# Kernel tuning notes

Measured on AMD Instinct MI355X. Metric: run time of the kernel, lower is better.

The kernel has to match this reference:

```python
import math
import jax, jax.numpy as jnp
import numpy as np

HIDDEN = 768
N_SIGNALS = 15
DIM = HIDDEN // 4  # 192
B, S = 32, 4096


def setup_inputs() -> dict:
    key = jax.random.key(0)
    ks = jax.random.split(key, 11)
    return {
        "token_embeds": jax.random.normal(ks[0], (B, S, HIDDEN), jnp.float32),
        "Wk": jax.random.normal(ks[1], (HIDDEN, DIM), jnp.float32) * 0.02,
        "bk": jax.random.normal(ks[2], (DIM,), jnp.float32) * 0.02,
        "Wv": jax.random.normal(ks[3], (HIDDEN, DIM), jnp.float32) * 0.02,
        "bv": jax.random.normal(ks[4], (DIM,), jnp.float32) * 0.02,
        "signal_queries": jax.random.normal(ks[5], (N_SIGNALS, DIM), jnp.float32),
        "null_embeddings": jax.random.normal(ks[6], (N_SIGNALS, HIDDEN), jnp.float32) * 0.01,
        "W1": jax.random.normal(ks[7], (2 * DIM, 64), jnp.float32) * 0.05,
        "b1": jax.random.normal(ks[8], (64,), jnp.float32) * 0.05,
        "W2": jax.random.normal(ks[9], (64, 1), jnp.float32) * 0.05,
        "b2": jax.random.normal(ks[10], (1,), jnp.float32) * 0.05,
    }


def reference(token_embeds, Wk, bk, Wv, bv, signal_queries, null_embeddings, W1, b1, W2, b2):
    b, s, h = token_embeds.shape
    d = Wk.shape[1]
    # detect_signals: cross-attention from signal queries to tokens
    keys = token_embeds @ Wk + bk        # [B,S,d]
    values = token_embeds @ Wv + bv      # [B,S,d]
    scale = jnp.sqrt(jnp.float32(d))
    attn = jnp.einsum("nd,bsd->bns", signal_queries, keys) / scale  # [B,N,S]
    attn_weights = jax.nn.softmax(attn, axis=-1)
    signal_embeds = jnp.einsum("bns,bsd->bnd", attn_weights, values)  # [B,N,d]
    entropy = -(attn_weights * jnp.log(attn_weights + 1e-10)).sum(-1)  # [B,N]
    strength = 1.0 - entropy / jnp.float32(math.log(s))
    # estimate_causal_effects: batched over the 15 signals (original loops in Python)
    null_proj = jnp.broadcast_to(null_embeddings[:, :d], (b, null_embeddings.shape[0], d))
    eff_in = jnp.concatenate([signal_embeds, null_proj], axis=-1)  # [B,N,2d]
    hdn = jax.nn.gelu(eff_in @ W1 + b1, approximate=False)
    effects = (hdn @ W2 + b2)[..., 0]  # [B,N]
    # package (effects, strength) as one array [B, 2N]
    return jnp.concatenate([effects, strength], axis=-1)
```

## Files before the change

### kernel.cpp

```cpp
#include <hip/hip_runtime.h>
#include <math.h>

#define HID   768
#define DIMD  192
#define NSIG  15
#define BB    32
#define SS    4096
#define INV_SCALE 0.07216878364870322f
#define LOG_S     8.31776616671934f
#define NCHUNK 16
#define SC     256

#define WS_QK    ((size_t)0)
#define WS_QB    (WS_QK + NSIG*HID)
#define WS_ATTN  (WS_QB + 64)
#define WS_M     (WS_ATTN + (size_t)BB*NSIG*SS)
#define WS_INVL  (WS_M + BB*NSIG)
#define WS_CTXP  (WS_INVL + BB*NSIG)

__global__ __launch_bounds__(256) void k_qk(const float* __restrict__ q,
                                            const float* __restrict__ Wk,
                                            const float* __restrict__ bk,
                                            float* __restrict__ ws) {
  int idx = blockIdx.x * 256 + threadIdx.x;
  if (idx < NSIG * HID) {
    int n = idx / HID, h = idx - n * HID;
    const float* qr = q + n * DIMD;
    const float* wr = Wk + h * DIMD;
    float s = 0.f;
    #pragma unroll 4
    for (int d = 0; d < DIMD; ++d) s = fmaf(qr[d], wr[d], s);
    ws[WS_QK + (size_t)n * HID + h] = s * INV_SCALE;
  }
  if (idx < NSIG) {
    const float* qr = q + idx * DIMD;
    float s = 0.f;
    for (int d = 0; d < DIMD; ++d) s = fmaf(qr[d], bk[d], s);
    ws[WS_QB + idx] = s * INV_SCALE;
  }
}

#define HC 16
__global__ __launch_bounds__(256) void k_logits(const float* __restrict__ X,
                                                const float* __restrict__ ws_qk,
                                                const float* __restrict__ ws_qb,
                                                float* __restrict__ attn) {
  __shared__ float Qs[NSIG * HID];
  __shared__ float Xs[256 * (HC + 1)];
  const int t  = threadIdx.x;
  const int s0 = blockIdx.x * 256;
  const int b  = blockIdx.y;

  #pragma unroll
  for (int k = 0; k < (NSIG * HID) / 256; ++k)
    Qs[t + k * 256] = ws_qk[t + k * 256];

  float acc[NSIG];
  #pragma unroll
  for (int n = 0; n < NSIG; ++n) acc[n] = ws_qb[n];

  const float* Xb = X + ((size_t)(b * SS + s0)) * HID;

  for (int c = 0; c < HID / HC; ++c) {
    __syncthreads();
    #pragma unroll
    for (int k = 0; k < 4; ++k) {
      int j  = t + k * 256;
      int r  = j >> 2, cc = j & 3;
      float4 xv = *(const float4*)(Xb + (size_t)r * HID + c * HC + cc * 4);
      float* dst = Xs + r * (HC + 1) + cc * 4;
      dst[0] = xv.x; dst[1] = xv.y; dst[2] = xv.z; dst[3] = xv.w;
    }
    __syncthreads();
    const float* xrow = Xs + t * (HC + 1);
    #pragma unroll
    for (int c4 = 0; c4 < HC / 4; ++c4) {
      float x0 = xrow[c4*4+0], x1 = xrow[c4*4+1], x2 = xrow[c4*4+2], x3 = xrow[c4*4+3];
      #pragma unroll
      for (int n = 0; n < NSIG; ++n) {
        float4 qv = *(const float4*)(Qs + n * HID + c * HC + c4 * 4);
        acc[n] = fmaf(x0, qv.x, acc[n]);
        acc[n] = fmaf(x1, qv.y, acc[n]);
        acc[n] = fmaf(x2, qv.z, acc[n]);
        acc[n] = fmaf(x3, qv.w, acc[n]);
      }
    }
  }
  #pragma unroll
  for (int n = 0; n < NSIG; ++n)
    attn[((size_t)(b * NSIG + n)) * SS + s0 + t] = acc[n];
}

__global__ __launch_bounds__(256) void k_softmax_stats(const float* __restrict__ attn,
                                                       float* __restrict__ m_out,
                                                       float* __restrict__ invl_out,
                                                       float* __restrict__ out) {
  const int blk = blockIdx.x;
  const int b = blk / NSIG, n = blk - b * NSIG;
  const float* row = attn + ((size_t)(b * NSIG + n)) * SS;
  const int t = threadIdx.x;
  __shared__ float red[8];

  float m = -1e30f;
  for (int i = t; i < SS; i += 256) m = fmaxf(m, row[i]);
  #pragma unroll
  for (int o = 32; o > 0; o >>= 1) m = fmaxf(m, __shfl_down(m, o, 64));
  if ((t & 63) == 0) red[t >> 6] = m;
  __syncthreads();
  m = fmaxf(fmaxf(red[0], red[1]), fmaxf(red[2], red[3]));

  float l = 0.f, pa = 0.f;
  for (int i = t; i < SS; i += 256) {
    float a = row[i];
    float e = expf(a - m);
    l += e; pa = fmaf(e, a, pa);
  }
  #pragma unroll
  for (int o = 32; o > 0; o >>= 1) { l += __shfl_down(l, o, 64); pa += __shfl_down(pa, o, 64); }
  __syncthreads();
  if ((t & 63) == 0) { red[t >> 6] = l; red[4 + (t >> 6)] = pa; }
  __syncthreads();
  if (t == 0) {
    float L  = red[0] + red[1] + red[2] + red[3];
    float PA = red[4] + red[5] + red[6] + red[7];
    float entropy = m + logf(L) - PA / L;
    m_out[blk]    = m;
    invl_out[blk] = 1.f / L;
    out[b * (2 * NSIG) + NSIG + n] = 1.f - entropy / LOG_S;
  }
}

__global__ __launch_bounds__(256) void k_ctx(const float* __restrict__ X,
                                             const float* __restrict__ attn,
                                             const float* __restrict__ m_arr,
                                             const float* __restrict__ invl_arr,
                                             float* __restrict__ ctxp) {
  __shared__ float wLDS[NSIG * SC];
  const int t = threadIdx.x;
  const int chunk = blockIdx.x, b = blockIdx.y;
  const int s0 = chunk * SC;

  #pragma unroll
  for (int n = 0; n < NSIG; ++n) {
    float a = attn[((size_t)(b * NSIG + n)) * SS + s0 + t];
    wLDS[n * SC + t] = expf(a - m_arr[b * NSIG + n]) * invl_arr[b * NSIG + n];
  }
  __syncthreads();

  float acc[NSIG * 3];
  #pragma unroll
  for (int i = 0; i < NSIG * 3; ++i) acc[i] = 0.f;

  const float* Xb = X + ((size_t)(b * SS + s0)) * HID + t;
  for (int s = 0; s < SC; s += 4) {
    float x[12];
    #pragma unroll
    for (int j = 0; j < 4; ++j)
      #pragma unroll
      for (int k = 0; k < 3; ++k)
        x[j * 3 + k] = Xb[(size_t)(s + j) * HID + k * 256];
    #pragma unroll
    for (int n = 0; n < NSIG; ++n) {
      float4 wv = *(const float4*)(wLDS + n * SC + s);
      float wa[4] = {wv.x, wv.y, wv.z, wv.w};
      #pragma unroll
      for (int j = 0; j < 4; ++j)
        #pragma unroll
        for (int k = 0; k < 3; ++k)
          acc[n * 3 + k] = fmaf(wa[j], x[j * 3 + k], acc[n * 3 + k]);
    }
  }
  float* dst = ctxp + ((size_t)((b * NCHUNK + chunk) * NSIG)) * HID;
  #pragma unroll
  for (int n = 0; n < NSIG; ++n)
    #pragma unroll
    for (int k = 0; k < 3; ++k)
      dst[(size_t)n * HID + k * 256 + t] = acc[n * 3 + k];
}

__global__ __launch_bounds__(256) void k_final(const float* __restrict__ ctxp,
                                               const float* __restrict__ Wv,
                                               const float* __restrict__ bv,
                                               const float* __restrict__ nullemb,
                                               const float* __restrict__ W1,
                                               const float* __restrict__ b1,
                                               const float* __restrict__ W2,
                                               const float* __restrict__ b2,
                                               float* __restrict__ out) {
  const int blk = blockIdx.x;
  const int b = blk / NSIG, n = blk - b * NSIG;
  const int t = threadIdx.x;
  __shared__ float ctx[HID];
  __shared__ float se[DIMD];

  #pragma unroll
  for (int k = 0; k < 3; ++k) {
    int h = t + k * 256;
    float s = 0.f;
    #pragma unroll 4
    for (int c = 0; c < NCHUNK; ++c)
      s += ctxp[((size_t)((b * NCHUNK + c) * NSIG + n)) * HID + h];
    ctx[h] = s;
  }
  __syncthreads();
  if (t < DIMD) {
    float s = bv[t];
    #pragma unroll 4
    for (int h = 0; h < HID; ++h)
      s = fmaf(ctx[h], Wv[(size_t)h * DIMD + t], s);
    se[t] = s;
  }
  __syncthreads();
  if (t < 64) {
    float s = b1[t];
    const float* nrow = nullemb + (size_t)n * HID;
    #pragma unroll 4
    for (int i = 0; i < DIMD; ++i) s = fmaf(se[i],   W1[(size_t)i * 64 + t], s);
    #pragma unroll 4
    for (int i = 0; i < DIMD; ++i) s = fmaf(nrow[i], W1[(size_t)(DIMD + i) * 64 + t], s);
    float g = 0.5f * s * (1.f + erff(s * 0.70710678118654752f));
    float val = g * W2[t];
    #pragma unroll
    for (int o = 32; o > 0; o >>= 1) val += __shfl_down(val, o, 64);
    if (t == 0) out[b * (2 * NSIG) + n] = val + b2[0];
  }
}

extern "C" void kernel_launch(void* const* d_in, const int* in_sizes, int n_in,
                              void* d_out, int out_size, void* d_ws, size_t ws_size,
                              hipStream_t stream) {
  const float* X   = (const float*)d_in[0];
  const float* Wk  = (const float*)d_in[1];
  const float* bk  = (const float*)d_in[2];
  const float* Wv  = (const float*)d_in[3];
  const float* bv  = (const float*)d_in[4];
  const float* q   = (const float*)d_in[5];
  const float* nul = (const float*)d_in[6];
  const float* W1  = (const float*)d_in[7];
  const float* b1  = (const float*)d_in[8];
  const float* W2  = (const float*)d_in[9];
  const float* b2  = (const float*)d_in[10];
  float* out = (float*)d_out;
  float* ws  = (float*)d_ws;

  hipLaunchKernelGGL(k_qk, dim3(45), dim3(256), 0, stream, q, Wk, bk, ws);
  hipLaunchKernelGGL(k_logits, dim3(SS / 256, BB), dim3(256), 0, stream,
                     X, ws + WS_QK, ws + WS_QB, ws + WS_ATTN);
  hipLaunchKernelGGL(k_softmax_stats, dim3(BB * NSIG), dim3(256), 0, stream,
                     ws + WS_ATTN, ws + WS_M, ws + WS_INVL, out);
  hipLaunchKernelGGL(k_ctx, dim3(NCHUNK, BB), dim3(256), 0, stream,
                     X, ws + WS_ATTN, ws + WS_M, ws + WS_INVL, ws + WS_CTXP);
  hipLaunchKernelGGL(k_final, dim3(BB * NSIG), dim3(256), 0, stream,
                     ws + WS_CTXP, Wv, bv, nul, W1, b1, W2, b2, out);
}
```

Measured before the change: 876.1 us.

## Fuse logits, softmax and context into one flash-style chunked kernel

Merges the logits, softmax-statistics and weighted-context kernels into a single kernel per (chunk, batch). Each chunk keeps its logits in registers and shared memory, computes local max/sum/entropy partials, and writes unnormalised partial contexts. The final kernel rescales the partials with an online-softmax combine. This removes the global attention-logit buffer round trip and two launches, and lets X for a chunk be reused from cache between the two passes. In exchange, the Q matrix is now read straight from global/cache rather than staged in shared memory, and the grid is limited to 512 blocks.

```diff
diff --git a/kernel.cpp b/kernel.cpp
--- a/kernel.cpp
+++ b/kernel.cpp
@@ -6,17 +6,16 @@
 #define NSIG  15
 #define BB    32
 #define SS    4096
+#define SC    256
+#define NCHUNK (SS / SC)
+#define HC    32
 #define INV_SCALE 0.07216878364870322f
 #define LOG_S     8.31776616671934f
-#define NCHUNK 16
-#define SC     256
-
-#define WS_QK    ((size_t)0)
-#define WS_QB    (WS_QK + NSIG*HID)
-#define WS_ATTN  (WS_QB + 64)
-#define WS_M     (WS_ATTN + (size_t)BB*NSIG*SS)
-#define WS_INVL  (WS_M + BB*NSIG)
-#define WS_CTXP  (WS_INVL + BB*NSIG)
+
+#define WS_QK   ((size_t)0)
+#define WS_QB   (WS_QK + NSIG * HID)
+#define WS_ST   (WS_QB + 16)
+#define WS_CTXP (WS_ST + (size_t)BB * NCHUNK * NSIG * 3)
 
 __global__ __launch_bounds__(256) void k_qk(const float* __restrict__ q,
                                             const float* __restrict__ Wk,
@@ -40,145 +39,117 @@
   }
 }
 
-#define HC 16
-__global__ __launch_bounds__(256) void k_logits(const float* __restrict__ X,
-                                                const float* __restrict__ ws_qk,
-                                                const float* __restrict__ ws_qb,
-                                                float* __restrict__ attn) {
-  __shared__ float Qs[NSIG * HID];
-  __shared__ float Xs[256 * (HC + 1)];
-  const int t  = threadIdx.x;
-  const int s0 = blockIdx.x * 256;
-  const int b  = blockIdx.y;
-
-  #pragma unroll
-  for (int k = 0; k < (NSIG * HID) / 256; ++k)
-    Qs[t + k * 256] = ws_qk[t + k * 256];
-
-  float acc[NSIG];
-  #pragma unroll
-  for (int n = 0; n < NSIG; ++n) acc[n] = ws_qb[n];
-
-  const float* Xb = X + ((size_t)(b * SS + s0)) * HID;
-
-  for (int c = 0; c < HID / HC; ++c) {
-    __syncthreads();
-    #pragma unroll
-    for (int k = 0; k < 4; ++k) {
-      int j  = t + k * 256;
-      int r  = j >> 2, cc = j & 3;
-      float4 xv = *(const float4*)(Xb + (size_t)r * HID + c * HC + cc * 4);
-      float* dst = Xs + r * (HC + 1) + cc * 4;
-      dst[0] = xv.x; dst[1] = xv.y; dst[2] = xv.z; dst[3] = xv.w;
-    }
-    __syncthreads();
-    const float* xrow = Xs + t * (HC + 1);
-    #pragma unroll
-    for (int c4 = 0; c4 < HC / 4; ++c4) {
-      float x0 = xrow[c4*4+0], x1 = xrow[c4*4+1], x2 = xrow[c4*4+2], x3 = xrow[c4*4+3];
-      #pragma unroll
-      for (int n = 0; n < NSIG; ++n) {
-        float4 qv = *(const float4*)(Qs + n * HID + c * HC + c4 * 4);
-        acc[n] = fmaf(x0, qv.x, acc[n]);
-        acc[n] = fmaf(x1, qv.y, acc[n]);
-        acc[n] = fmaf(x2, qv.z, acc[n]);
-        acc[n] = fmaf(x3, qv.w, acc[n]);
-      }
-    }
-  }
-  #pragma unroll
-  for (int n = 0; n < NSIG; ++n)
-    attn[((size_t)(b * NSIG + n)) * SS + s0 + t] = acc[n];
-}
-
-__global__ __launch_bounds__(256) void k_softmax_stats(const float* __restrict__ attn,
-                                                       float* __restrict__ m_out,
-                                                       float* __restrict__ invl_out,
-                                                       float* __restrict__ out) {
-  const int blk = blockIdx.x;
-  const int b = blk / NSIG, n = blk - b * NSIG;
-  const float* row = attn + ((size_t)(b * NSIG + n)) * SS;
-  const int t = threadIdx.x;
-  __shared__ float red[8];
-
-  float m = -1e30f;
-  for (int i = t; i < SS; i += 256) m = fmaxf(m, row[i]);
-  #pragma unroll
-  for (int o = 32; o > 0; o >>= 1) m = fmaxf(m, __shfl_down(m, o, 64));
-  if ((t & 63) == 0) red[t >> 6] = m;
-  __syncthreads();
-  m = fmaxf(fmaxf(red[0], red[1]), fmaxf(red[2], red[3]));
-
-  float l = 0.f, pa = 0.f;
-  for (int i = t; i < SS; i += 256) {
-    float a = row[i];
-    float e = expf(a - m);
-    l += e; pa = fmaf(e, a, pa);
-  }
-  #pragma unroll
-  for (int o = 32; o > 0; o >>= 1) { l += __shfl_down(l, o, 64); pa += __shfl_down(pa, o, 64); }
-  __syncthreads();
-  if ((t & 63) == 0) { red[t >> 6] = l; red[4 + (t >> 6)] = pa; }
-  __syncthreads();
-  if (t == 0) {
-    float L  = red[0] + red[1] + red[2] + red[3];
-    float PA = red[4] + red[5] + red[6] + red[7];
-    float entropy = m + logf(L) - PA / L;
-    m_out[blk]    = m;
-    invl_out[blk] = 1.f / L;
-    out[b * (2 * NSIG) + NSIG + n] = 1.f - entropy / LOG_S;
-  }
-}
-
-__global__ __launch_bounds__(256) void k_ctx(const float* __restrict__ X,
-                                             const float* __restrict__ attn,
-                                             const float* __restrict__ m_arr,
-                                             const float* __restrict__ invl_arr,
-                                             float* __restrict__ ctxp) {
-  __shared__ float wLDS[NSIG * SC];
+__global__ __launch_bounds__(256) void k_fused(const float* __restrict__ X,
+                                               const float* __restrict__ qk,
+                                               const float* __restrict__ qb,
+                                               float* __restrict__ stats,
+                                               float* __restrict__ ctxp) {
+  __shared__ float smem[SC * (HC + 1)];
   const int t = threadIdx.x;
   const int chunk = blockIdx.x, b = blockIdx.y;
   const int s0 = chunk * SC;
-
+  const float* Xb = X + ((size_t)(b * SS + s0)) * HID;
+
+  float acc[NSIG];
+  #pragma unroll
+  for (int n = 0; n < NSIG; ++n) acc[n] = qb[n];
+
+  for (int c = 0; c < HID / HC; ++c) {
+    __syncthreads();
+    #pragma unroll
+    for (int k = 0; k < 8; ++k) {
+      int j = t + k * 256;
+      int r = j >> 3, cc = j & 7;
+      float4 xv = *(const float4*)(Xb + (size_t)r * HID + c * HC + cc * 4);
+      float* dst = smem + r * (HC + 1) + cc * 4;
+      dst[0] = xv.x; dst[1] = xv.y; dst[2] = xv.z; dst[3] = xv.w;
+    }
+    __syncthreads();
+    const float* xrow = smem + t * (HC + 1);
+    float x[HC];
+    #pragma unroll
+    for (int j = 0; j < HC; ++j) x[j] = xrow[j];
+    const float* Qc = qk + c * HC;
+    #pragma unroll
+    for (int n = 0; n < NSIG; ++n) {
+      const float* Qn = Qc + (size_t)n * HID;
+      float s = 0.f;
+      #pragma unroll
+      for (int j = 0; j < HC; ++j) s = fmaf(x[j], Qn[j], s);
+      acc[n] += s;
+    }
+  }
+
+  const int wv = t >> 6;
+  float mloc[NSIG];
   #pragma unroll
   for (int n = 0; n < NSIG; ++n) {
-    float a = attn[((size_t)(b * NSIG + n)) * SS + s0 + t];
-    wLDS[n * SC + t] = expf(a - m_arr[b * NSIG + n]) * invl_arr[b * NSIG + n];
-  }
-  __syncthreads();
-
-  float acc[NSIG * 3];
-  #pragma unroll
-  for (int i = 0; i < NSIG * 3; ++i) acc[i] = 0.f;
-
-  const float* Xb = X + ((size_t)(b * SS + s0)) * HID + t;
+    float v = acc[n];
+    #pragma unroll
+    for (int o = 32; o > 0; o >>= 1) v = fmaxf(v, __shfl_xor(v, o, 64));
+    mloc[n] = v;
+  }
+  __syncthreads();
+  float* wS   = smem;
+  float* redM = smem + NSIG * SC;
+  float* redL = redM + NSIG * 4;
+  float* redP = redL + NSIG * 4;
+  if ((t & 63) == 0) {
+    #pragma unroll
+    for (int n = 0; n < NSIG; ++n) redM[n * 4 + wv] = mloc[n];
+  }
+  __syncthreads();
+  #pragma unroll
+  for (int n = 0; n < NSIG; ++n) {
+    float m = fmaxf(fmaxf(redM[n*4+0], redM[n*4+1]), fmaxf(redM[n*4+2], redM[n*4+3]));
+    float e = expf(acc[n] - m);
+    wS[n * SC + t] = e;
+    float l = e, pa = e * acc[n];
+    #pragma unroll
+    for (int o = 32; o > 0; o >>= 1) { l += __shfl_xor(l, o, 64); pa += __shfl_xor(pa, o, 64); }
+    if ((t & 63) == 0) { redL[n * 4 + wv] = l; redP[n * 4 + wv] = pa; }
+  }
+  __syncthreads();
+  if (t < NSIG) {
+    float m  = fmaxf(fmaxf(redM[t*4+0], redM[t*4+1]), fmaxf(redM[t*4+2], redM[t*4+3]));
+    float l  = redL[t*4+0] + redL[t*4+1] + redL[t*4+2] + redL[t*4+3];
+    float pa = redP[t*4+0] + redP[t*4+1] + redP[t*4+2] + redP[t*4+3];
+    float* st = stats + ((size_t)((b * NCHUNK + chunk) * NSIG + t)) * 3;
+    st[0] = m; st[1] = l; st[2] = pa;
+  }
+
+  float accB[NSIG * 3];
+  #pragma unroll
+  for (int i = 0; i < NSIG * 3; ++i) accB[i] = 0.f;
+  const float* Xc = Xb + t;
   for (int s = 0; s < SC; s += 4) {
     float x[12];
     #pragma unroll
     for (int j = 0; j < 4; ++j)
       #pragma unroll
       for (int k = 0; k < 3; ++k)
-        x[j * 3 + k] = Xb[(size_t)(s + j) * HID + k * 256];
+        x[j * 3 + k] = Xc[(size_t)(s + j) * HID + k * 256];
     #pragma unroll
     for (int n = 0; n < NSIG; ++n) {
-      float4 wv = *(const float4*)(wLDS + n * SC + s);
-      float wa[4] = {wv.x, wv.y, wv.z, wv.w};
+      float4 w4 = *(const float4*)(wS + n * SC + s);
+      float wa[4] = {w4.x, w4.y, w4.z, w4.w};
       #pragma unroll
       for (int j = 0; j < 4; ++j)
         #pragma unroll
         for (int k = 0; k < 3; ++k)
-          acc[n * 3 + k] = fmaf(wa[j], x[j * 3 + k], acc[n * 3 + k]);
-    }
-  }
-  float* dst = ctxp + ((size_t)((b * NCHUNK + chunk) * NSIG)) * HID;
+          accB[n * 3 + k] = fmaf(wa[j], x[j * 3 + k], accB[n * 3 + k]);
+    }
+  }
+  float* dst = ctxp + ((size_t)((b * NCHUNK + chunk) * NSIG)) * HID + t;
   #pragma unroll
   for (int n = 0; n < NSIG; ++n)
     #pragma unroll
     for (int k = 0; k < 3; ++k)
-      dst[(size_t)n * HID + k * 256 + t] = acc[n * 3 + k];
-}
-
-__global__ __launch_bounds__(256) void k_final(const float* __restrict__ ctxp,
+      dst[(size_t)n * HID + k * 256] = accB[n * 3 + k];
+}
+
+__global__ __launch_bounds__(256) void k_final(const float* __restrict__ stats,
+                                               const float* __restrict__ ctxp,
                                                const float* __restrict__ Wv,
                                                const float* __restrict__ bv,
                                                const float* __restrict__ nullemb,
@@ -190,19 +161,43 @@
   const int blk = blockIdx.x;
   const int b = blk / NSIG, n = blk - b * NSIG;
   const int t = threadIdx.x;
+  __shared__ float alpha[NCHUNK];
   __shared__ float ctx[HID];
   __shared__ float se[DIMD];
+
+  if (t == 0) {
+    float mc[NCHUNK], lc[NCHUNK], pc[NCHUNK];
+    float m = -1e30f;
+    #pragma unroll
+    for (int c = 0; c < NCHUNK; ++c) {
+      const float* st = stats + ((size_t)((b * NCHUNK + c) * NSIG + n)) * 3;
+      mc[c] = st[0]; lc[c] = st[1]; pc[c] = st[2];
+      m = fmaxf(m, mc[c]);
+    }
+    float L = 0.f, PA = 0.f;
+    #pragma unroll
+    for (int c = 0; c < NCHUNK; ++c) {
+      float scl = expf(mc[c] - m);
+      L = fmaf(scl, lc[c], L); PA = fmaf(scl, pc[c], PA);
+    }
+    #pragma unroll
+    for (int c = 0; c < NCHUNK; ++c) alpha[c] = expf(mc[c] - m) / L;
+    float entropy = m + logf(L) - PA / L;
+    out[b * (2 * NSIG) + NSIG + n] = 1.f - entropy / LOG_S;
+  }
+  __syncthreads();
 
   #pragma unroll
   for (int k = 0; k < 3; ++k) {
     int h = t + k * 256;
     float s = 0.f;
-    #pragma unroll 4
+    #pragma unroll
     for (int c = 0; c < NCHUNK; ++c)
-      s += ctxp[((size_t)((b * NCHUNK + c) * NSIG + n)) * HID + h];
+      s = fmaf(alpha[c], ctxp[((size_t)((b * NCHUNK + c) * NSIG + n)) * HID + h], s);
     ctx[h] = s;
   }
   __syncthreads();
+
   if (t < DIMD) {
     float s = bv[t];
     #pragma unroll 4
@@ -211,6 +206,7 @@
     se[t] = s;
   }
   __syncthreads();
+
   if (t < 64) {
     float s = b1[t];
     const float* nrow = nullemb + (size_t)n * HID;
@@ -244,12 +240,8 @@
   float* ws  = (float*)d_ws;
 
   hipLaunchKernelGGL(k_qk, dim3(45), dim3(256), 0, stream, q, Wk, bk, ws);
-  hipLaunchKernelGGL(k_logits, dim3(SS / 256, BB), dim3(256), 0, stream,
-                     X, ws + WS_QK, ws + WS_QB, ws + WS_ATTN);
-  hipLaunchKernelGGL(k_softmax_stats, dim3(BB * NSIG), dim3(256), 0, stream,
-                     ws + WS_ATTN, ws + WS_M, ws + WS_INVL, out);
-  hipLaunchKernelGGL(k_ctx, dim3(NCHUNK, BB), dim3(256), 0, stream,
-                     X, ws + WS_ATTN, ws + WS_M, ws + WS_INVL, ws + WS_CTXP);
+  hipLaunchKernelGGL(k_fused, dim3(NCHUNK, BB), dim3(256), 0, stream,
+                     X, ws + WS_QK, ws + WS_QB, ws + WS_ST, ws + WS_CTXP);
   hipLaunchKernelGGL(k_final, dim3(BB * NSIG), dim3(256), 0, stream,
-                     ws + WS_CTXP, Wv, bv, nul, W1, b1, W2, b2, out);
-}
+                     ws + WS_ST, ws + WS_CTXP, Wv, bv, nul, W1, b1, W2, b2, out);
+}
```

Result: no change. 893.5 us (+2.0%).
